# Kernel optimization log

Measured on AMD Instinct MI355X. Metric: run time of the kernel, lower is better.

The kernel has to match this reference:

```python
import jax, jax.numpy as jnp
import numpy as np


def _seg_softmax(e, seg, n):
    m = jax.ops.segment_max(e, seg, num_segments=n)
    ex = jnp.exp(e - m[seg])
    s = jax.ops.segment_sum(ex, seg, num_segments=n)
    return ex / (s[seg] + 1e-16)


def _gat_conv(x, src, dst, ea, W, a_s, a_d, We, a_e, b, heads, C, concat, N):
    # PyG GATConv math (eval mode, no dropout)
    h = (x @ W).reshape(N, heads, C)                    # [N,H,C]
    he = (ea @ We).reshape(-1, heads, C)                # [Ef,H,C]
    al = jnp.sum(h * a_s, -1)[src] + jnp.sum(h * a_d, -1)[dst] + jnp.sum(he * a_e, -1)
    al = jax.nn.leaky_relu(al, 0.2)                     # [Ef,H]
    alpha = _seg_softmax(al, dst, N)
    out = jax.ops.segment_sum(alpha[:, :, None] * h[src], dst, num_segments=N)
    out = out.reshape(N, heads * C) if concat else out.mean(1)
    return out + b


def _ln(x, g, b):
    mu = x.mean(-1, keepdims=True)
    v = x.var(-1, keepdims=True)
    return (x - mu) / jnp.sqrt(v + 1e-5) * g + b


def setup_inputs() -> dict:
    key = jax.random.key(0)
    ks = jax.random.split(key, 20)
    B, L, E_PER = 512, 64, 4
    N = B * L
    E = N * E_PER
    x = jax.random.normal(ks[0], (N, 55), jnp.float32)
    # within-graph random edges (each graph is a contiguous block of L nodes)
    off = (jnp.arange(E) // (L * E_PER)) * L
    src = off + jax.random.randint(ks[1], (E,), 0, L)
    dst = off + jax.random.randint(ks[2], (E,), 0, L)
    edge_index = jnp.stack([src, dst])
    edge_attr = jax.random.uniform(ks[3], (E, 6), dtype=jnp.float32)
    node_gid = jnp.arange(N) // L
    food_ids = jax.random.randint(ks[4], (B,), 0, 29)
    p = lambda i, shape: jax.random.normal(ks[i], shape, jnp.float32) * 0.05
    return dict(
        x=x, edge_attr=edge_attr, edge_index=edge_index, node_gid=node_gid, food_ids=food_ids,
        W1=p(5, (55, 1024)), as1=p(6, (4, 256)), ad1=p(7, (4, 256)),
        We1=p(8, (6, 1024)), ae1=p(9, (4, 256)), b1=jnp.zeros((1024,), jnp.float32),
        g1=jnp.ones((1024,), jnp.float32), be1=jnp.zeros((1024,), jnp.float32),
        W2=p(10, (1024, 256)), as2=p(11, (1, 256)), ad2=p(12, (1, 256)),
        We2=p(13, (6, 256)), ae2=p(14, (1, 256)), b2=jnp.zeros((256,), jnp.float32),
        g2=jnp.ones((256,), jnp.float32), be2=jnp.zeros((256,), jnp.float32),
        Wa=p(15, (256, 256)), va=p(16, (256,)), emb=p(17, (29, 256)))


def reference(x, edge_attr, edge_index, node_gid, food_ids,
              W1, as1, ad1, We1, ae1, b1, g1, be1,
              W2, as2, ad2, We2, ae2, b2, g2, be2,
              Wa, va, emb):
    N = x.shape[0]
    B = food_ids.shape[0]
    src, dst = edge_index[0], edge_index[1]
    # add self loops; self-loop edge_attr = mean of incoming edge attrs (PyG fill_value='mean')
    ones = jnp.ones((src.shape[0],), x.dtype)
    deg = jax.ops.segment_sum(ones, dst, num_segments=N)
    mean_ea = jax.ops.segment_sum(edge_attr, dst, num_segments=N) / jnp.maximum(deg, 1.0)[:, None]
    loop = jnp.arange(N)
    src_f = jnp.concatenate([src, loop])
    dst_f = jnp.concatenate([dst, loop])
    ea_f = jnp.concatenate([edge_attr, mean_ea], 0)
    # GATEncoder
    h = _gat_conv(x, src_f, dst_f, ea_f, W1, as1, ad1, We1, ae1, b1, 4, 256, True, N)
    h = jax.nn.relu(_ln(h, g1, be1))
    h = _gat_conv(h, src_f, dst_f, ea_f, W2, as2, ad2, We2, ae2, b2, 1, 256, False, N)
    h = _ln(h, g2, be2)                                  # [N,256]
    # per-graph attention over nodes, then attention-weighted max-pool
    scores = jnp.tanh(h @ Wa) @ va                       # [N]
    attn = _seg_softmax(scores, node_gid, B)             # [N]
    hw = h * attn[:, None]
    drug_fea = jax.ops.segment_max(hw, node_gid, num_segments=B)[:, None, :]  # [B,1,256]
    food_fea = emb[food_ids][:, None, :]                 # [B,1,256]
    return drug_fea, food_fea, attn
```

## Files before the change

### kernel.cpp

```cpp
#include <hip/hip_runtime.h>
#include <cstdint>
#include <cstddef>


#define LEAKY_SLOPE 0.2f

typedef __attribute__((ext_vector_type(8))) _Float16 half8;
typedef __attribute__((ext_vector_type(4))) float facc4;

__global__ void k_prep_w(const float* __restrict__ W1, const float* __restrict__ W2,
                         const float* __restrict__ Wa,
                         const float* __restrict__ We1, const float* __restrict__ ae1,
                         const float* __restrict__ We2, const float* __restrict__ ae2,
                         const float* __restrict__ as1, const float* __restrict__ ad1,
                         const float* __restrict__ as2, const float* __restrict__ ad2,
                         _Float16* __restrict__ w1t, _Float16* __restrict__ w2t,
                         _Float16* __restrict__ wat, float* __restrict__ fold) {
    int idx = blockIdx.x * blockDim.x + threadIdx.x;
    if (idx < 1024 * 64) {
        int c = idx >> 6, k = idx & 63;
        w1t[idx] = (k < 55) ? (_Float16)W1[(size_t)k * 1024 + c] : (_Float16)0.f;
        return;
    }
    idx -= 1024 * 64;
    if (idx < 256 * 1024) {
        int c = idx >> 10, k = idx & 1023;
        w2t[idx] = (_Float16)W2[(size_t)k * 256 + c];
        return;
    }
    idx -= 256 * 1024;
    if (idx < 256 * 256) {
        int c = idx >> 8, k = idx & 255;
        int dst = ((c >> 4) * 8 + (k >> 5)) * 512 + ((c & 15) + 16 * ((k >> 3) & 3)) * 8 + (k & 7);
        wat[dst] = (_Float16)Wa[(size_t)k * 256 + c];
        return;
    }
    int t = idx - 256 * 256;
    if (t < 24) {
        int k = t >> 2, h = t & 3;
        float s = 0.f;
        for (int c = 0; c < 256; ++c) s += We1[k * 1024 + h * 256 + c] * ae1[h * 256 + c];
        fold[t] = s;
    } else if (t < 30) {
        int k = t - 24;
        float s = 0.f;
        for (int c = 0; c < 256; ++c) s += We2[k * 256 + c] * ae2[c];
        fold[32 + k] = s;
    } else if (t >= 64 && t < 284) {
        int i = t - 64, k = i >> 2, h = i & 3;
        float s = 0.f;
        for (int c = 0; c < 256; ++c) s += W1[k * 1024 + h * 256 + c] * as1[h * 256 + c];
        fold[64 + i] = s;
    } else if (t >= 320 && t < 540) {
        int i = t - 320, k = i >> 2, h = i & 3;
        float s = 0.f;
        for (int c = 0; c < 256; ++c) s += W1[k * 1024 + h * 256 + c] * ad1[h * 256 + c];
        fold[320 + i] = s;
    } else if (t >= 1024 && t < 2048) {
        int k = t - 1024;
        float s = 0.f;
        for (int c = 0; c < 256; ++c) s += W2[k * 256 + c] * as2[c];
        fold[1024 + k] = s;
    } else if (t >= 2048 && t < 3072) {
        int k = t - 2048;
        float s = 0.f;
        for (int c = 0; c < 256; ++c) s += W2[k * 256 + c] * ad2[c];
        fold[2048 + k] = s;
    }
}

__global__ void k_prep_x(const float* __restrict__ x, const float* __restrict__ wa1,
                         const float* __restrict__ wd1, _Float16* __restrict__ xbf,
                         float* __restrict__ ss1, float* __restrict__ sd1, int N) {
    int idx = blockIdx.x * blockDim.x + threadIdx.x;
    if (idx < N * 64) {
        int n = idx >> 6, k = idx & 63;
        _Float16 v = (k < 55) ? (_Float16)x[(size_t)n * 55 + k] : (_Float16)0.f;
        int g = n >> 6, nl = n & 63;
        size_t dst = (size_t)g * 4096 +
                     (((k >> 4) * 2 + (nl >> 5)) * 512 +
                      ((k & 15) + 16 * ((nl >> 3) & 3)) * 8 + (nl & 7));
        xbf[dst] = v;
        return;
    }
    int n = idx - N * 64;
    if (n >= N) return;
    float a0 = 0, a1 = 0, a2 = 0, a3 = 0, d0 = 0, d1 = 0, d2 = 0, d3 = 0;
    for (int k = 0; k < 55; ++k) {
        float xv = x[(size_t)n * 55 + k];
        float4 wa = *reinterpret_cast<const float4*>(&wa1[k * 4]);
        float4 wd = *reinterpret_cast<const float4*>(&wd1[k * 4]);
        a0 += xv * wa.x; a1 += xv * wa.y; a2 += xv * wa.z; a3 += xv * wa.w;
        d0 += xv * wd.x; d1 += xv * wd.y; d2 += xv * wd.z; d3 += xv * wd.w;
    }
    *reinterpret_cast<float4*>(&ss1[n * 4]) = make_float4(a0, a1, a2, a3);
    *reinterpret_cast<float4*>(&sd1[n * 4]) = make_float4(d0, d1, d2, d3);
}

__global__ __launch_bounds__(256) void k_graph_csr(
    const int* __restrict__ ei, const float* __restrict__ ea,
    const float* __restrict__ we1, const float* __restrict__ we2,
    int* __restrict__ coff, int* __restrict__ eid,
    float* __restrict__ ead1, float* __restrict__ ead2, int E, int B) {
    __shared__ int degL[64];
    __shared__ float meaL[64][6];
    __shared__ int cs[65];
    __shared__ int fillL[64];
    int g = blockIdx.x;
    int ng = g * 64;
    int e0 = g * 256;
    int tid = threadIdx.x;
    if (tid < 64) {
        degL[tid] = 0; fillL[tid] = 0;
#pragma unroll
        for (int k = 0; k < 6; ++k) meaL[tid][k] = 0.f;
    }
    __syncthreads();
    int eg = e0 + tid;
    int dst = ei[E + eg];
    int dl = dst - ng;
    atomicAdd(&degL[dl], 1);
#pragma unroll
    for (int k = 0; k < 6; ++k) atomicAdd(&meaL[dl][k], ea[(size_t)eg * 6 + k]);
    __syncthreads();
    if (tid < 64) {
        int v = degL[tid] + 1;
        int incl = v;
#pragma unroll
        for (int o = 1; o < 64; o <<= 1) {
            int up = __shfl_up(incl, o);
            if (tid >= o) incl += up;
        }
        cs[tid + 1] = incl;
        if (tid == 0) cs[0] = 0;
        coff[ng + tid] = g * 320 + (incl - v);
        if (g == B - 1 && tid == 63) coff[ng + 64] = (g + 1) * 320;
    }
    __syncthreads();
    {
        float v[4] = {};
        float v2 = 0.f;
        const float* eap = ea + (size_t)eg * 6;
#pragma unroll
        for (int k = 0; k < 6; ++k) {
            float a = eap[k];
#pragma unroll
            for (int h = 0; h < 4; ++h) v[h] += a * we1[k * 4 + h];
            v2 += a * we2[k];
        }
#pragma unroll
        for (int h = 0; h < 4; ++h) ead1[(size_t)eg * 4 + h] = v[h];
        ead2[eg] = v2;
        int pos = cs[dl] + atomicAdd(&fillL[dl], 1);
        eid[g * 320 + pos] = eg;
    }
    if (tid < 64) {
        float inv = 1.f / fmaxf((float)degL[tid], 1.f);
        float v[4] = {};
        float v2 = 0.f;
#pragma unroll
        for (int k = 0; k < 6; ++k) {
            float a = meaL[tid][k] * inv;
#pragma unroll
            for (int h = 0; h < 4; ++h) v[h] += a * we1[k * 4 + h];
            v2 += a * we2[k];
        }
        int se = E + ng + tid;
#pragma unroll
        for (int h = 0; h < 4; ++h) ead1[(size_t)se * 4 + h] = v[h];
        ead2[se] = v2;
        int pos = cs[tid] + atomicAdd(&fillL[tid], 1);
        eid[g * 320 + pos] = se;
    }
}

__global__ __launch_bounds__(512) void k_pbuild1(
    const _Float16* __restrict__ xbf,
    const int* __restrict__ coff, const int* __restrict__ eid, const int* __restrict__ ei,
    const float* __restrict__ ead1, const float* __restrict__ ss1,
    const float* __restrict__ sd1,
    _Float16* __restrict__ XA, int ldxa, int E, int g0) {
    __shared__ _Float16 Pm[4][64 * 64];
    __shared__ float llds[384][4];
    __shared__ int slds[384];
    int g = blockIdx.x;
    int ng = (g0 + g) * 64;
    int lr0 = g * 64;
    int tid = threadIdx.x;
    int lane = tid & 63, wid = tid >> 6;
    int l15 = lane & 15, l4 = lane >> 4;
    for (int i = tid; i < 4 * 64 * 64 / 8; i += 512)
        *reinterpret_cast<int4*>(&Pm[0][0] + i * 8) = int4{0, 0, 0, 0};
    int pbase = coff[ng];
    int pcnt = coff[ng + 64] - pbase;
    if (pcnt > 384) pcnt = 384;
    for (int p = tid; p < pcnt; p += 512) {
        int e = eid[pbase + p];
        int s, d;
        if (e < E) { s = ei[e]; d = ei[E + e]; } else { s = e - E; d = s; }
        slds[p] = s - ng;
        float4 sv = *reinterpret_cast<const float4*>(&ss1[s * 4]);
        float4 dv = *reinterpret_cast<const float4*>(&sd1[d * 4]);
        float4 ev = *reinterpret_cast<const float4*>(&ead1[(size_t)e * 4]);
        float v0 = sv.x + dv.x + ev.x, v1 = sv.y + dv.y + ev.y;
        float v2 = sv.z + dv.z + ev.z, v3 = sv.w + dv.w + ev.w;
        llds[p][0] = (v0 > 0.f) ? v0 : LEAKY_SLOPE * v0;
        llds[p][1] = (v1 > 0.f) ? v1 : LEAKY_SLOPE * v1;
        llds[p][2] = (v2 > 0.f) ? v2 : LEAKY_SLOPE * v2;
        llds[p][3] = (v3 > 0.f) ? v3 : LEAKY_SLOPE * v3;
    }
    __syncthreads();
    if (tid < 256) {
        int dst = tid >> 2, h = tid & 3;
        int p0 = coff[ng + dst] - pbase, p1 = coff[ng + dst + 1] - pbase;
        float m = -1e30f;
        for (int p = p0; p < p1; ++p) m = fmaxf(m, llds[p][h]);
        float sm = 0.f;
        for (int p = p0; p < p1; ++p) sm += expf(llds[p][h] - m);
        float iv = 1.f / (sm + 1e-16f);
        for (int p = p0; p < p1; ++p) {
            int src = slds[p];
            int pos = dst * 64 + (((src >> 3) ^ (dst & 7)) << 3) + (src & 7);
            Pm[h][pos] = (_Float16)((float)Pm[h][pos] + expf(llds[p][h] - m) * iv);
        }
    }
    __syncthreads();
    int head = wid >> 1, fjh = wid & 1;
    const _Float16* xg = xbf + (size_t)(g0 + g) * 4096;
    facc4 acc[4][2] = {};
#pragma unroll
    for (int kk = 0; kk < 2; ++kk) {
        half8 af[4], bf[2];
#pragma unroll
        for (int f = 0; f < 4; ++f) {
            int arow = f * 16 + l15;
            af[f] = *reinterpret_cast<const half8*>(
                &Pm[head][arow * 64 + (((kk * 4 + l4) ^ (arow & 7)) << 3)]);
        }
#pragma unroll
        for (int f = 0; f < 2; ++f)
            bf[f] = *reinterpret_cast<const half8*>(
                xg + (((fjh * 2 + f) * 2 + kk) * 512 + lane * 8));
#pragma unroll
        for (int fi = 0; fi < 4; ++fi)
#pragma unroll
            for (int fj = 0; fj < 2; ++fj)
                acc[fi][fj] = __builtin_amdgcn_mfma_f32_16x16x32_f16(
                    af[fi], bf[fj], acc[fi][fj], 0, 0, 0);
    }
#pragma unroll
    for (int fi = 0; fi < 4; ++fi)
#pragma unroll
        for (int fj = 0; fj < 2; ++fj)
#pragma unroll
            for (int i = 0; i < 4; ++i) {
                int r = fi * 16 + l4 * 4 + i;
                int k2 = fjh * 32 + fj * 16 + l15;
                XA[((size_t)head * ldxa + lr0 + r) * 64 + k2] = (_Float16)acc[fi][fj][i];
            }
}

__global__ __launch_bounds__(256) void k_gemm_heads(
    const _Float16* __restrict__ XA, int ldxa, const _Float16* __restrict__ w1t,
    _Float16* __restrict__ hpre) {
    int h = blockIdx.z;
    const _Float16* A = XA + (size_t)h * ldxa * 64;
    const _Float16* BT = w1t + (size_t)h * 256 * 64;
    __shared__ _Float16 As[128 * 64];
    __shared__ _Float16 Bs[128 * 64];
    int tid = threadIdx.x;
    int lane = tid & 63, wid = tid >> 6;
    int wr = wid >> 1, wc = wid & 1;
    int l15 = lane & 15, l4 = lane >> 4;
    int r0 = blockIdx.y * 128, c0 = blockIdx.x * 128;
    facc4 acc[4][4] = {};
#pragma unroll
    for (int i = 0; i < 4; ++i) {
        int ch = tid + 256 * i;
        int row = ch >> 3, col16 = ch & 7;
        int sw = col16 ^ (row & 7);
        *reinterpret_cast<int4*>(&As[row * 64 + sw * 8]) =
            *reinterpret_cast<const int4*>(A + (size_t)(r0 + row) * 64 + col16 * 8);
        *reinterpret_cast<int4*>(&Bs[row * 64 + sw * 8]) =
            *reinterpret_cast<const int4*>(BT + (size_t)(c0 + row) * 64 + col16 * 8);
    }
    __syncthreads();
#pragma unroll
    for (int kk = 0; kk < 2; ++kk) {
        half8 af[4], bf[4];
#pragma unroll
        for (int f = 0; f < 4; ++f) {
            int arow = wr * 64 + f * 16 + l15;
            int ac = (kk * 4 + l4) ^ (arow & 7);
            af[f] = *reinterpret_cast<const half8*>(&As[arow * 64 + ac * 8]);
            int brow = wc * 64 + f * 16 + l15;
            int bc = (kk * 4 + l4) ^ (brow & 7);
            bf[f] = *reinterpret_cast<const half8*>(&Bs[brow * 64 + bc * 8]);
        }
#pragma unroll
        for (int fi = 0; fi < 4; ++fi)
#pragma unroll
            for (int fj = 0; fj < 4; ++fj)
                acc[fi][fj] = __builtin_amdgcn_mfma_f32_16x16x32_f16(
                    af[fi], bf[fj], acc[fi][fj], 0, 0, 0);
    }
#pragma unroll
    for (int fi = 0; fi < 4; ++fi)
#pragma unroll
        for (int fj = 0; fj < 4; ++fj)
#pragma unroll
            for (int i = 0; i < 4; ++i) {
                int r = r0 + wr * 64 + fi * 16 + l4 * 4 + i;
                int cc = h * 256 + c0 + wc * 64 + fj * 16 + l15;
                hpre[(size_t)r * 1024 + cc] = (_Float16)acc[fi][fj][i];
            }
}

__global__ __launch_bounds__(256) void k_ln1(
    const _Float16* __restrict__ hpre, const float* __restrict__ b1,
    const float* __restrict__ g1, const float* __restrict__ be1,
    const float* __restrict__ w2a, const float* __restrict__ w2d,
    _Float16* __restrict__ hln, float* __restrict__ ss2, float* __restrict__ sd2,
    int n0) {
    int row = blockIdx.x * 4 + (threadIdx.x >> 6);
    int lane = threadIdx.x & 63;
    const _Float16* src = hpre + (size_t)row * 1024;
    float v[16];
    half8 h0 = *reinterpret_cast<const half8*>(src + lane * 8);
    half8 h1 = *reinterpret_cast<const half8*>(src + 512 + lane * 8);
    float lsum = 0.f, lsq = 0.f;
#pragma unroll
    for (int j = 0; j < 8; ++j) {
        v[j] = (float)h0[j] + b1[lane * 8 + j];
        v[8 + j] = (float)h1[j] + b1[512 + lane * 8 + j];
    }
#pragma unroll
    for (int j = 0; j < 16; ++j) { lsum += v[j]; lsq += v[j] * v[j]; }
    for (int o = 32; o; o >>= 1) { lsum += __shfl_xor(lsum, o); lsq += __shfl_xor(lsq, o); }
    float mu = lsum * (1.f / 1024.f);
    float var = lsq * (1.f / 1024.f) - mu * mu;
    float rstd = rsqrtf(var + 1e-5f);
    float s2 = 0.f, d2 = 0.f;
    half8 o0, o1;
#pragma unroll
    for (int j = 0; j < 8; ++j) {
        int c = lane * 8 + j;
        float t = fmaxf((v[j] - mu) * rstd * g1[c] + be1[c], 0.f);
        o0[j] = (_Float16)t;
        s2 += t * w2a[c]; d2 += t * w2d[c];
    }
#pragma unroll
    for (int j = 0; j < 8; ++j) {
        int c = 512 + lane * 8 + j;
        float t = fmaxf((v[8 + j] - mu) * rstd * g1[c] + be1[c], 0.f);
        o1[j] = (_Float16)t;
        s2 += t * w2a[c]; d2 += t * w2d[c];
    }
    *reinterpret_cast<half8*>(hln + (size_t)row * 1024 + lane * 8) = o0;
    *reinterpret_cast<half8*>(hln + (size_t)row * 1024 + 512 + lane * 8) = o1;
    for (int o = 32; o; o >>= 1) { s2 += __shfl_xor(s2, o); d2 += __shfl_xor(d2, o); }
    if (lane == 0) { ss2[n0 + row] = s2; sd2[n0 + row] = d2; }
}

__global__ __launch_bounds__(256) void k_gemm2(
    const _Float16* __restrict__ A, const _Float16* __restrict__ BT,
    _Float16* __restrict__ C, int ldc) {
    __shared__ _Float16 As[128 * 64];
    __shared__ _Float16 Bs[128 * 64];
    int tid = threadIdx.x;
    int lane = tid & 63, wid = tid >> 6;
    int wr = wid >> 1, wc = wid & 1;
    int l15 = lane & 15, l4 = lane >> 4;
    int r0 = blockIdx.y * 128, c0 = blockIdx.x * 128;
    facc4 acc[4][4] = {};
    for (int kt = 0; kt < 1024; kt += 64) {
#pragma unroll
        for (int i = 0; i < 4; ++i) {
            int ch = tid + 256 * i;
            int row = ch >> 3, col16 = ch & 7;
            int sw = col16 ^ (row & 7);
            *reinterpret_cast<int4*>(&As[row * 64 + sw * 8]) =
                *reinterpret_cast<const int4*>(A + (size_t)(r0 + row) * 1024 + kt + col16 * 8);
            *reinterpret_cast<int4*>(&Bs[row * 64 + sw * 8]) =
                *reinterpret_cast<const int4*>(BT + (size_t)(c0 + row) * 1024 + kt + col16 * 8);
        }
        __syncthreads();
#pragma unroll
        for (int kk = 0; kk < 2; ++kk) {
            half8 af[4], bf[4];
#pragma unroll
            for (int f = 0; f < 4; ++f) {
                int arow = wr * 64 + f * 16 + l15;
                int ac = (kk * 4 + l4) ^ (arow & 7);
                af[f] = *reinterpret_cast<const half8*>(&As[arow * 64 + ac * 8]);
                int brow = wc * 64 + f * 16 + l15;
                int bc = (kk * 4 + l4) ^ (brow & 7);
                bf[f] = *reinterpret_cast<const half8*>(&Bs[brow * 64 + bc * 8]);
            }
#pragma unroll
            for (int fi = 0; fi < 4; ++fi)
#pragma unroll
                for (int fj = 0; fj < 4; ++fj)
                    acc[fi][fj] = __builtin_amdgcn_mfma_f32_16x16x32_f16(
                        af[fi], bf[fj], acc[fi][fj], 0, 0, 0);
        }
        __syncthreads();
    }
#pragma unroll
    for (int fi = 0; fi < 4; ++fi)
#pragma unroll
        for (int fj = 0; fj < 4; ++fj)
#pragma unroll
            for (int i = 0; i < 4; ++i) {
                int r = r0 + wr * 64 + fi * 16 + l4 * 4 + i;
                int cc = c0 + wc * 64 + fj * 16 + l15;
                C[(size_t)r * ldc + cc] = (_Float16)acc[fi][fj][i];
            }
}

__global__ __launch_bounds__(512) void k_graph2(
    const _Float16* __restrict__ h2t, int ldh,
    const int* __restrict__ coff, const int* __restrict__ eid, const int* __restrict__ ei,
    const float* __restrict__ ead2, const float* __restrict__ ss2,
    const float* __restrict__ sd2,
    const float* __restrict__ b2, const float* __restrict__ g2,
    const float* __restrict__ be2,
    float* __restrict__ hfc, _Float16* __restrict__ hfb, int E, int g0) {
    __shared__ _Float16 Pm[64 * 64];
    __shared__ float llds[384];
    __shared__ int slds[384];
    __shared__ float rsum[64], rsq[64];
    int g = blockIdx.x;
    int ng = (g0 + g) * 64;
    int lr0 = g * 64;
    int tid = threadIdx.x;
    int lane = tid & 63, wid = tid >> 6;
    int l15 = lane & 15, l4 = lane >> 4;
    if (tid < 64) { rsum[tid] = 0.f; rsq[tid] = 0.f; }
    for (int i = tid; i < 64 * 64 / 8; i += 512)
        *reinterpret_cast<int4*>(&Pm[0] + i * 8) = int4{0, 0, 0, 0};
    int pbase = coff[ng];
    int pcnt = coff[ng + 64] - pbase;
    if (pcnt > 384) pcnt = 384;
    for (int p = tid; p < pcnt; p += 512) {
        int e = eid[pbase + p];
        int s, d;
        if (e < E) { s = ei[e]; d = ei[E + e]; } else { s = e - E; d = s; }
        slds[p] = s - ng;
        float v = ss2[s] + sd2[d] + ead2[e];
        llds[p] = (v > 0.f) ? v : LEAKY_SLOPE * v;
    }
    __syncthreads();
    if (tid < 64) {
        int dst = tid;
        int p0 = coff[ng + dst] - pbase, p1 = coff[ng + dst + 1] - pbase;
        float m = -1e30f;
        for (int p = p0; p < p1; ++p) m = fmaxf(m, llds[p]);
        float sm = 0.f;
        for (int p = p0; p < p1; ++p) sm += expf(llds[p] - m);
        float iv = 1.f / (sm + 1e-16f);
        for (int p = p0; p < p1; ++p) {
            int src = slds[p];
            int pos = dst * 64 + (((src >> 3) ^ (dst & 7)) << 3) + (src & 7);
            Pm[pos] = (_Float16)((float)Pm[pos] + expf(llds[p] - m) * iv);
        }
    }
    __syncthreads();
    facc4 acc[4][2] = {};
    int cbase = wid * 32;
#pragma unroll
    for (int kk = 0; kk < 2; ++kk) {
        half8 af[4], bf[2];
#pragma unroll
        for (int f = 0; f < 4; ++f) {
            int arow = f * 16 + l15;
            af[f] = *reinterpret_cast<const half8*>(
                &Pm[arow * 64 + (((kk * 4 + l4) ^ (arow & 7)) << 3)]);
        }
#pragma unroll
        for (int f = 0; f < 2; ++f) {
            int c = cbase + f * 16 + l15;
            bf[f] = *reinterpret_cast<const half8*>(
                h2t + (size_t)c * ldh + lr0 + kk * 32 + l4 * 8);
        }
#pragma unroll
        for (int fi = 0; fi < 4; ++fi)
#pragma unroll
            for (int fj = 0; fj < 2; ++fj)
                acc[fi][fj] = __builtin_amdgcn_mfma_f32_16x16x32_f16(
                    af[fi], bf[fj], acc[fi][fj], 0, 0, 0);
    }
    float bb[2];
#pragma unroll
    for (int fj = 0; fj < 2; ++fj) bb[fj] = b2[cbase + fj * 16 + l15];
#pragma unroll
    for (int fi = 0; fi < 4; ++fi)
#pragma unroll
        for (int i = 0; i < 4; ++i) {
            float s = 0.f, q = 0.f;
#pragma unroll
            for (int fj = 0; fj < 2; ++fj) {
                float v = acc[fi][fj][i] + bb[fj];
                acc[fi][fj][i] = v;
                s += v; q += v * v;
            }
            s += __shfl_xor(s, 1); q += __shfl_xor(q, 1);
            s += __shfl_xor(s, 2); q += __shfl_xor(q, 2);
            s += __shfl_xor(s, 4); q += __shfl_xor(q, 4);
            s += __shfl_xor(s, 8); q += __shfl_xor(q, 8);
            if (l15 == 0) {
                int r = fi * 16 + l4 * 4 + i;
                atomicAdd(&rsum[r], s);
                atomicAdd(&rsq[r], q);
            }
        }
    __syncthreads();
#pragma unroll
    for (int fi = 0; fi < 4; ++fi)
#pragma unroll
        for (int i = 0; i < 4; ++i) {
            int r = fi * 16 + l4 * 4 + i;
            float mu = rsum[r] * (1.f / 256.f);
            float var = rsq[r] * (1.f / 256.f) - mu * mu;
            float rstd = rsqrtf(var + 1e-5f);
#pragma unroll
            for (int fj = 0; fj < 2; ++fj) {
                int c = cbase + fj * 16 + l15;
                float v = (acc[fi][fj][i] - mu) * rstd * g2[c] + be2[c];
                hfc[(size_t)(lr0 + r) * 256 + c] = v;
                size_t dst = (size_t)g * 16384 +
                             ((fi * 8 + (c >> 5)) * 512 +
                              ((r & 15) + 16 * ((c >> 3) & 3)) * 8 + (c & 7));
                hfb[dst] = (_Float16)v;
            }
        }
}

__global__ __launch_bounds__(512) void k_scores_final(
    const _Float16* __restrict__ hfb, const _Float16* __restrict__ wat,
    const float* __restrict__ va, const float* __restrict__ hfc,
    const int* __restrict__ food, const float* __restrict__ emb,
    float* __restrict__ out, int B, int g0) {
    __shared__ float part[8][64];
    __shared__ float at[64];
    __shared__ float pmax[2][256];
    int g = blockIdx.x;
    int b = g0 + g;
    int r0 = g * 64;
    int tid = threadIdx.x;
    int lane = tid & 63, wid = tid >> 6;
    int l15 = lane & 15, l4 = lane >> 4;
    int cbase = wid * 32;
    const _Float16* hg = hfb + (size_t)g * 16384;
    facc4 acc[4][2] = {};
#pragma unroll
    for (int kk = 0; kk < 8; ++kk) {
        half8 af[4], bf[2];
#pragma unroll
        for (int f = 0; f < 4; ++f)
            af[f] = *reinterpret_cast<const half8*>(hg + ((f * 8 + kk) * 512 + lane * 8));
#pragma unroll
        for (int f = 0; f < 2; ++f)
            bf[f] = *reinterpret_cast<const half8*>(
                wat + (((wid * 2 + f) * 8 + kk) * 512 + lane * 8));
#pragma unroll
        for (int fi = 0; fi < 4; ++fi)
#pragma unroll
            for (int fj = 0; fj < 2; ++fj)
                acc[fi][fj] = __builtin_amdgcn_mfma_f32_16x16x32_f16(
                    af[fi], bf[fj], acc[fi][fj], 0, 0, 0);
    }
    float vac[2];
#pragma unroll
    for (int fj = 0; fj < 2; ++fj) vac[fj] = va[cbase + fj * 16 + l15];
#pragma unroll
    for (int fi = 0; fi < 4; ++fi)
#pragma unroll
        for (int i = 0; i < 4; ++i) {
            float v = tanhf(acc[fi][0][i]) * vac[0] + tanhf(acc[fi][1][i]) * vac[1];
            v += __shfl_xor(v, 1); v += __shfl_xor(v, 2);
            v += __shfl_xor(v, 4); v += __shfl_xor(v, 8);
            if (l15 == 0) part[wid][fi * 16 + l4 * 4 + i] = v;
        }
    __syncthreads();
    if (tid < 64) {
        float sc = part[0][tid] + part[1][tid] + part[2][tid] + part[3][tid] +
                   part[4][tid] + part[5][tid] + part[6][tid] + part[7][tid];
        float m = sc;
        for (int o = 32; o; o >>= 1) m = fmaxf(m, __shfl_xor(m, o));
        float ex = expf(sc - m);
        float s = ex;
        for (int o = 32; o; o >>= 1) s += __shfl_xor(s, o);
        float a = ex / (s + 1e-16f);
        at[tid] = a;
        out[(size_t)B * 512 + (size_t)b * 64 + tid] = a;
    }
    __syncthreads();
    {
        int c = tid & 255, half = tid >> 8;
        float m = -1e30f;
        for (int l = half * 32; l < half * 32 + 32; ++l)
            m = fmaxf(m, hfc[(size_t)(r0 + l) * 256 + c] * at[l]);
        pmax[half][c] = m;
    }
    __syncthreads();
    if (tid < 256) {
        out[(size_t)b * 256 + tid] = fmaxf(pmax[0][tid], pmax[1][tid]);
        out[(size_t)B * 256 + (size_t)b * 256 + tid] =
            emb[(size_t)food[b] * 256 + tid];
    }
}

extern "C" void kernel_launch(void* const* d_in, const int* in_sizes, int n_in,
                              void* d_out, int out_size, void* d_ws, size_t ws_size,
                              hipStream_t stream) {
    const float* x   = (const float*)d_in[0];
    const float* ea  = (const float*)d_in[1];
    const int*   ei  = (const int*)d_in[2];
    const int*   food= (const int*)d_in[4];
    const float* W1  = (const float*)d_in[5];
    const float* as1 = (const float*)d_in[6];
    const float* ad1 = (const float*)d_in[7];
    const float* We1 = (const float*)d_in[8];
    const float* ae1 = (const float*)d_in[9];
    const float* b1  = (const float*)d_in[10];
    const float* g1  = (const float*)d_in[11];
    const float* be1 = (const float*)d_in[12];
    const float* W2  = (const float*)d_in[13];
    const float* as2 = (const float*)d_in[14];
    const float* ad2 = (const float*)d_in[15];
    const float* We2 = (const float*)d_in[16];
    const float* ae2 = (const float*)d_in[17];
    const float* b2  = (const float*)d_in[18];
    const float* g2  = (const float*)d_in[19];
    const float* be2 = (const float*)d_in[20];
    const float* Wa  = (const float*)d_in[21];
    const float* va  = (const float*)d_in[22];
    const float* emb = (const float*)d_in[23];
    float* out = (float*)d_out;

    const int N  = in_sizes[0] / 55;
    const int E  = in_sizes[2] / 2;
    const int B  = in_sizes[4];
    const int Ef = E + N;
    const int LPG = N / B;

    char* w = (char*)d_ws;
    size_t off = 0;
    auto take = [&](size_t bytes) -> char* {
        char* p = w + off;
        off = (off + bytes + 255) & ~(size_t)255;
        return p;
    };
    int*      coff = (int*)take((size_t)(N + 1) * 4);
    int*      eid  = (int*)take((size_t)Ef * 4);
    float*    ead1 = (float*)take((size_t)Ef * 4 * 4);
    float*    ead2 = (float*)take((size_t)Ef * 4);
    float*    fold = (float*)take(4096 * 4);
    float*    ss1  = (float*)take((size_t)N * 4 * 4);
    float*    sd1  = (float*)take((size_t)N * 4 * 4);
    float*    ss2  = (float*)take((size_t)N * 4);
    float*    sd2  = (float*)take((size_t)N * 4);
    _Float16* xbf  = (_Float16*)take((size_t)N * 64 * 2);
    _Float16* w1t  = (_Float16*)take((size_t)1024 * 64 * 2);
    _Float16* w2t  = (_Float16*)take((size_t)256 * 1024 * 2);
    _Float16* wat  = (_Float16*)take((size_t)256 * 256 * 2);
    size_t smallEnd = off;

    int G = B;
    while (G > 2 && smallEnd + (size_t)G * 32768 + 2ull * G * 131072 + 768 > ws_size) G >>= 1;
    _Float16* XA   = (_Float16*)take((size_t)G * 32768);
    _Float16* hpre = (_Float16*)take((size_t)G * 131072);
    _Float16* hln  = (_Float16*)take((size_t)G * 131072);
    _Float16* h2t = hpre;
    float*    hfc = (float*)((char*)hpre + (size_t)G * 32768);
    _Float16* hfb = (_Float16*)((char*)hpre + (size_t)G * 98304);

    k_prep_w<<<(1024 * 64 + 256 * 1024 + 256 * 256 + 3072 + 255) / 256, 256, 0, stream>>>(
        W1, W2, Wa, We1, ae1, We2, ae2, as1, ad1, as2, ad2, w1t, w2t, wat, fold);
    k_prep_x<<<(N * 64 + N + 255) / 256, 256, 0, stream>>>(
        x, fold + 64, fold + 320, xbf, ss1, sd1, N);
    k_graph_csr<<<B, 256, 0, stream>>>(ei, ea, fold, fold + 32, coff, eid,
                                       ead1, ead2, E, B);

    for (int g0 = 0; g0 < B; g0 += G) {
        int Gc = (g0 + G <= B) ? G : (B - g0);
        int n0 = g0 * LPG;
        int NC = Gc * LPG;
        k_pbuild1<<<Gc, 512, 0, stream>>>(xbf, coff, eid, ei, ead1, ss1, sd1,
                                          XA, NC, E, g0);
        k_gemm_heads<<<dim3(2, NC / 128, 4), 256, 0, stream>>>(XA, NC, w1t, hpre);
        k_ln1<<<NC / 4, 256, 0, stream>>>(hpre, b1, g1, be1, fold + 1024, fold + 2048,
                                          hln, ss2, sd2, n0);
        k_gemm2<<<dim3(NC / 128, 2), 256, 0, stream>>>(w2t, hln, h2t, NC);
        k_graph2<<<Gc, 512, 0, stream>>>(h2t, NC, coff, eid, ei, ead2, ss2, sd2,
                                         b2, g2, be2, hfc, hfb, E, g0);
        k_scores_final<<<Gc, 512, 0, stream>>>(hfb, wat, va, hfc, food, emb,
                                               out, B, g0);
    }
}
```

Baseline: 164.5 us.

## Compute layer-2 attention logits in graph kernel and widen GEMM2 tiles

Removes the folded W2·as2/W2·ad2 precompute and the per-row dot products in the LayerNorm kernel. The graph2 kernel instead computes source and destination scores from the GEMM2 output it already loads, using shared-memory atomics. GEMM2 is restructured so each 512-thread block covers all 256 output columns for 128 rows. Its output is written in a per-graph fragment layout that graph2 reads directly as MFMA operands. This trims work in ln1, gives graph2 coalesced fragment loads, and cuts the folding work in prep. The cost is extra fp16-precision reductions inside graph2 and a larger GEMM2 block with 48 KB of shared memory.

```diff
diff --git a/kernel.cpp b/kernel.cpp
--- a/kernel.cpp
+++ b/kernel.cpp
@@ -13,7 +13,6 @@
                          const float* __restrict__ We1, const float* __restrict__ ae1,
                          const float* __restrict__ We2, const float* __restrict__ ae2,
                          const float* __restrict__ as1, const float* __restrict__ ad1,
-                         const float* __restrict__ as2, const float* __restrict__ ad2,
                          _Float16* __restrict__ w1t, _Float16* __restrict__ w2t,
                          _Float16* __restrict__ wat, float* __restrict__ fold) {
     int idx = blockIdx.x * blockDim.x + threadIdx.x;
@@ -56,16 +55,6 @@
         float s = 0.f;
         for (int c = 0; c < 256; ++c) s += W1[k * 1024 + h * 256 + c] * ad1[h * 256 + c];
         fold[320 + i] = s;
-    } else if (t >= 1024 && t < 2048) {
-        int k = t - 1024;
-        float s = 0.f;
-        for (int c = 0; c < 256; ++c) s += W2[k * 256 + c] * as2[c];
-        fold[1024 + k] = s;
-    } else if (t >= 2048 && t < 3072) {
-        int k = t - 2048;
-        float s = 0.f;
-        for (int c = 0; c < 256; ++c) s += W2[k * 256 + c] * ad2[c];
-        fold[2048 + k] = s;
     }
 }
 
@@ -319,9 +308,7 @@
 __global__ __launch_bounds__(256) void k_ln1(
     const _Float16* __restrict__ hpre, const float* __restrict__ b1,
     const float* __restrict__ g1, const float* __restrict__ be1,
-    const float* __restrict__ w2a, const float* __restrict__ w2d,
-    _Float16* __restrict__ hln, float* __restrict__ ss2, float* __restrict__ sd2,
-    int n0) {
+    _Float16* __restrict__ hln) {
     int row = blockIdx.x * 4 + (threadIdx.x >> 6);
     int lane = threadIdx.x & 63;
     const _Float16* src = hpre + (size_t)row * 1024;
@@ -340,49 +327,48 @@
     float mu = lsum * (1.f / 1024.f);
     float var = lsq * (1.f / 1024.f) - mu * mu;
     float rstd = rsqrtf(var + 1e-5f);
-    float s2 = 0.f, d2 = 0.f;
     half8 o0, o1;
 #pragma unroll
     for (int j = 0; j < 8; ++j) {
         int c = lane * 8 + j;
-        float t = fmaxf((v[j] - mu) * rstd * g1[c] + be1[c], 0.f);
-        o0[j] = (_Float16)t;
-        s2 += t * w2a[c]; d2 += t * w2d[c];
+        o0[j] = (_Float16)fmaxf((v[j] - mu) * rstd * g1[c] + be1[c], 0.f);
     }
 #pragma unroll
     for (int j = 0; j < 8; ++j) {
         int c = 512 + lane * 8 + j;
-        float t = fmaxf((v[8 + j] - mu) * rstd * g1[c] + be1[c], 0.f);
-        o1[j] = (_Float16)t;
-        s2 += t * w2a[c]; d2 += t * w2d[c];
+        o1[j] = (_Float16)fmaxf((v[8 + j] - mu) * rstd * g1[c] + be1[c], 0.f);
     }
     *reinterpret_cast<half8*>(hln + (size_t)row * 1024 + lane * 8) = o0;
     *reinterpret_cast<half8*>(hln + (size_t)row * 1024 + 512 + lane * 8) = o1;
-    for (int o = 32; o; o >>= 1) { s2 += __shfl_xor(s2, o); d2 += __shfl_xor(d2, o); }
-    if (lane == 0) { ss2[n0 + row] = s2; sd2[n0 + row] = d2; }
-}
-
-__global__ __launch_bounds__(256) void k_gemm2(
+}
+
+__global__ __launch_bounds__(512) void k_gemm2(
     const _Float16* __restrict__ A, const _Float16* __restrict__ BT,
-    _Float16* __restrict__ C, int ldc) {
+    _Float16* __restrict__ h2f) {
     __shared__ _Float16 As[128 * 64];
-    __shared__ _Float16 Bs[128 * 64];
+    __shared__ _Float16 Bs[256 * 64];
     int tid = threadIdx.x;
     int lane = tid & 63, wid = tid >> 6;
-    int wr = wid >> 1, wc = wid & 1;
+    int wr = wid >> 2, wc = wid & 3;
     int l15 = lane & 15, l4 = lane >> 4;
-    int r0 = blockIdx.y * 128, c0 = blockIdx.x * 128;
+    int r0 = blockIdx.x * 128;
     facc4 acc[4][4] = {};
     for (int kt = 0; kt < 1024; kt += 64) {
 #pragma unroll
-        for (int i = 0; i < 4; ++i) {
-            int ch = tid + 256 * i;
+        for (int i = 0; i < 2; ++i) {
+            int ch = tid + 512 * i;
             int row = ch >> 3, col16 = ch & 7;
             int sw = col16 ^ (row & 7);
             *reinterpret_cast<int4*>(&As[row * 64 + sw * 8]) =
                 *reinterpret_cast<const int4*>(A + (size_t)(r0 + row) * 1024 + kt + col16 * 8);
+        }
+#pragma unroll
+        for (int i = 0; i < 4; ++i) {
+            int ch = tid + 512 * i;
+            int row = ch >> 3, col16 = ch & 7;
+            int sw = col16 ^ (row & 7);
             *reinterpret_cast<int4*>(&Bs[row * 64 + sw * 8]) =
-                *reinterpret_cast<const int4*>(BT + (size_t)(c0 + row) * 1024 + kt + col16 * 8);
+                *reinterpret_cast<const int4*>(BT + (size_t)row * 1024 + kt + col16 * 8);
         }
         __syncthreads();
 #pragma unroll
@@ -413,32 +399,76 @@
 #pragma unroll
             for (int i = 0; i < 4; ++i) {
                 int r = r0 + wr * 64 + fi * 16 + l4 * 4 + i;
-                int cc = c0 + wc * 64 + fj * 16 + l15;
-                C[(size_t)r * ldc + cc] = (_Float16)acc[fi][fj][i];
+                int cc = wc * 64 + fj * 16 + l15;
+                int g = r >> 6, nl = r & 63;
+                size_t dst = (size_t)g * 16384 +
+                             (((cc >> 4) * 2 + (nl >> 5)) * 512 +
+                              ((cc & 15) + 16 * ((nl >> 3) & 3)) * 8 + (nl & 7));
+                h2f[dst] = (_Float16)acc[fi][fj][i];
             }
 }
 
 __global__ __launch_bounds__(512) void k_graph2(
-    const _Float16* __restrict__ h2t, int ldh,
+    const _Float16* __restrict__ h2f,
     const int* __restrict__ coff, const int* __restrict__ eid, const int* __restrict__ ei,
-    const float* __restrict__ ead2, const float* __restrict__ ss2,
-    const float* __restrict__ sd2,
+    const float* __restrict__ ead2, const float* __restrict__ as2,
+    const float* __restrict__ ad2,
     const float* __restrict__ b2, const float* __restrict__ g2,
     const float* __restrict__ be2,
     float* __restrict__ hfc, _Float16* __restrict__ hfb, int E, int g0) {
     __shared__ _Float16 Pm[64 * 64];
     __shared__ float llds[384];
     __shared__ int slds[384];
-    __shared__ float rsum[64], rsq[64];
+    __shared__ float rsum[64], rsq[64], ss2L[64], sd2L[64];
     int g = blockIdx.x;
     int ng = (g0 + g) * 64;
     int lr0 = g * 64;
     int tid = threadIdx.x;
     int lane = tid & 63, wid = tid >> 6;
     int l15 = lane & 15, l4 = lane >> 4;
-    if (tid < 64) { rsum[tid] = 0.f; rsq[tid] = 0.f; }
+    int cbase = wid * 32;
+    if (tid < 64) { rsum[tid] = 0.f; rsq[tid] = 0.f; ss2L[tid] = 0.f; sd2L[tid] = 0.f; }
     for (int i = tid; i < 64 * 64 / 8; i += 512)
         *reinterpret_cast<int4*>(&Pm[0] + i * 8) = int4{0, 0, 0, 0};
+    __syncthreads();
+    const _Float16* hg = h2f + (size_t)g * 16384;
+    half8 bfr[2][2];
+#pragma unroll
+    for (int kk = 0; kk < 2; ++kk)
+#pragma unroll
+        for (int f = 0; f < 2; ++f)
+            bfr[kk][f] = *reinterpret_cast<const half8*>(
+                hg + ((((cbase + f * 16) >> 4) * 2 + kk) * 512 + lane * 8));
+    float ps[2][8] = {}, pd[2][8] = {};
+#pragma unroll
+    for (int kk = 0; kk < 2; ++kk)
+#pragma unroll
+        for (int f = 0; f < 2; ++f) {
+            int c = cbase + f * 16 + l15;
+            float a2 = as2[c], d2 = ad2[c];
+#pragma unroll
+            for (int j = 0; j < 8; ++j) {
+                float hv = (float)bfr[kk][f][j];
+                ps[kk][j] += hv * a2;
+                pd[kk][j] += hv * d2;
+            }
+        }
+#pragma unroll
+    for (int kk = 0; kk < 2; ++kk)
+#pragma unroll
+        for (int j = 0; j < 8; ++j) {
+            float s = ps[kk][j], d = pd[kk][j];
+            s += __shfl_xor(s, 1); d += __shfl_xor(d, 1);
+            s += __shfl_xor(s, 2); d += __shfl_xor(d, 2);
+            s += __shfl_xor(s, 4); d += __shfl_xor(d, 4);
+            s += __shfl_xor(s, 8); d += __shfl_xor(d, 8);
+            if (l15 == 0) {
+                int n = kk * 32 + l4 * 8 + j;
+                atomicAdd(&ss2L[n], s);
+                atomicAdd(&sd2L[n], d);
+            }
+        }
+    __syncthreads();
     int pbase = coff[ng];
     int pcnt = coff[ng + 64] - pbase;
     if (pcnt > 384) pcnt = 384;
@@ -447,7 +477,7 @@
         int s, d;
         if (e < E) { s = ei[e]; d = ei[E + e]; } else { s = e - E; d = s; }
         slds[p] = s - ng;
-        float v = ss2[s] + sd2[d] + ead2[e];
+        float v = ss2L[s - ng] + sd2L[d - ng] + ead2[e];
         llds[p] = (v > 0.f) ? v : LEAKY_SLOPE * v;
     }
     __syncthreads();
@@ -467,10 +497,9 @@
     }
     __syncthreads();
     facc4 acc[4][2] = {};
-    int cbase = wid * 32;
 #pragma unroll
     for (int kk = 0; kk < 2; ++kk) {
-        half8 af[4], bf[2];
+        half8 af[4];
 #pragma unroll
         for (int f = 0; f < 4; ++f) {
             int arow = f * 16 + l15;
@@ -478,17 +507,11 @@
                 &Pm[arow * 64 + (((kk * 4 + l4) ^ (arow & 7)) << 3)]);
         }
 #pragma unroll
-        for (int f = 0; f < 2; ++f) {
-            int c = cbase + f * 16 + l15;
-            bf[f] = *reinterpret_cast<const half8*>(
-                h2t + (size_t)c * ldh + lr0 + kk * 32 + l4 * 8);
-        }
-#pragma unroll
         for (int fi = 0; fi < 4; ++fi)
 #pragma unroll
             for (int fj = 0; fj < 2; ++fj)
                 acc[fi][fj] = __builtin_amdgcn_mfma_f32_16x16x32_f16(
-                    af[fi], bf[fj], acc[fi][fj], 0, 0, 0);
+                    af[fi], bfr[kk][fj], acc[fi][fj], 0, 0, 0);
     }
     float bb[2];
 #pragma unroll
@@ -659,8 +682,6 @@
     float*    fold = (float*)take(4096 * 4);
     float*    ss1  = (float*)take((size_t)N * 4 * 4);
     float*    sd1  = (float*)take((size_t)N * 4 * 4);
-    float*    ss2  = (float*)take((size_t)N * 4);
-    float*    sd2  = (float*)take((size_t)N * 4);
     _Float16* xbf  = (_Float16*)take((size_t)N * 64 * 2);
     _Float16* w1t  = (_Float16*)take((size_t)1024 * 64 * 2);
     _Float16* w2t  = (_Float16*)take((size_t)256 * 1024 * 2);
@@ -672,12 +693,12 @@
     _Float16* XA   = (_Float16*)take((size_t)G * 32768);
     _Float16* hpre = (_Float16*)take((size_t)G * 131072);
     _Float16* hln  = (_Float16*)take((size_t)G * 131072);
-    _Float16* h2t = hpre;
+    _Float16* h2f = (_Float16*)hpre;
     float*    hfc = (float*)((char*)hpre + (size_t)G * 32768);
     _Float16* hfb = (_Float16*)((char*)hpre + (size_t)G * 98304);
 
     k_prep_w<<<(1024 * 64 + 256 * 1024 + 256 * 256 + 3072 + 255) / 256, 256, 0, stream>>>(
-        W1, W2, Wa, We1, ae1, We2, ae2, as1, ad1, as2, ad2, w1t, w2t, wat, fold);
+        W1, W2, Wa, We1, ae1, We2, ae2, as1, ad1, w1t, w2t, wat, fold);
     k_prep_x<<<(N * 64 + N + 255) / 256, 256, 0, stream>>>(
         x, fold + 64, fold + 320, xbf, ss1, sd1, N);
     k_graph_csr<<<B, 256, 0, stream>>>(ei, ea, fold, fold + 32, coff, eid,
@@ -686,14 +707,14 @@
     for (int g0 = 0; g0 < B; g0 += G) {
         int Gc = (g0 + G <= B) ? G : (B - g0);
         int n0 = g0 * LPG;
+        (void)n0;
         int NC = Gc * LPG;
         k_pbuild1<<<Gc, 512, 0, stream>>>(xbf, coff, eid, ei, ead1, ss1, sd1,
                                           XA, NC, E, g0);
         k_gemm_heads<<<dim3(2, NC / 128, 4), 256, 0, stream>>>(XA, NC, w1t, hpre);
-        k_ln1<<<NC / 4, 256, 0, stream>>>(hpre, b1, g1, be1, fold + 1024, fold + 2048,
-                                          hln, ss2, sd2, n0);
-        k_gemm2<<<dim3(NC / 128, 2), 256, 0, stream>>>(w2t, hln, h2t, NC);
-        k_graph2<<<Gc, 512, 0, stream>>>(h2t, NC, coff, eid, ei, ead2, ss2, sd2,
+        k_ln1<<<NC / 4, 256, 0, stream>>>(hpre, b1, g1, be1, hln);
+        k_gemm2<<<NC / 128, 512, 0, stream>>>(hln, w2t, h2f);
+        k_graph2<<<Gc, 512, 0, stream>>>(h2f, coff, eid, ei, ead2, as2, ad2,
                                          b2, g2, be2, hfc, hfb, E, g0);
         k_scores_final<<<Gc, 512, 0, stream>>>(hfb, wat, va, hfc, food, emb,
                                                out, B, g0);
```

Result: no change. 163.1 us (-0.8%).
